# Kernel optimization log

Hardware: AMD Instinct MI355X
Metric: run time of the kernel (lower is better)

## Reference

```python
import jax, jax.numpy as jnp
import numpy as np

KERNEL = (3, 3, 3)
STRIDE = (1, 1, 1)
PAD = (1, 1, 1)
DIL = (1, 1, 1)


def setup_inputs() -> dict:
    key = jax.random.key(0)
    k1, k2 = jax.random.split(key)
    # input: [B, C, D, H, W]
    x = jax.random.normal(k1, (2, 64, 16, 64, 64), dtype=jnp.float32)
    # per-pixel weights: [B, heads, weight_channels, kernel_volume, D_out, H_out, W_out]
    weight = jax.random.normal(k2, (2, 1, 16, 27, 16, 64, 64), dtype=jnp.float32)
    return {"x": x, "weight": weight}


def _aggregate(x, weight):
    # involution-style 3D local aggregation with zero padding.
    B, C, D, H, W = x.shape
    _, heads, wc, kvol, Do, Ho, Wo = weight.shape
    kd, kh, kw = KERNEL
    assert kvol == kd * kh * kw and C % wc == 0
    Q = C // wc  # channel-sharing groups: channel c uses weight channel c % wc
    xp = jnp.pad(x, ((0, 0), (0, 0), (PAD[0], PAD[0]), (PAD[1], PAD[1]), (PAD[2], PAD[2])))
    # channels laid out so that c = q*wc + r -> weight channel r == c % wc
    out = jnp.zeros((B, heads, Q, wc, Do, Ho, Wo), dtype=x.dtype)
    for ikd in range(kd):
        for ikh in range(kh):
            for ikw in range(kw):  # fixed small structural loop (27 taps)
                k = (ikd * kh + ikh) * kw + ikw
                d0 = ikd * DIL[0]
                h0 = ikh * DIL[1]
                w0 = ikw * DIL[2]
                x_k = xp[:, :,
                         d0:d0 + (Do - 1) * STRIDE[0] + 1:STRIDE[0],
                         h0:h0 + (Ho - 1) * STRIDE[1] + 1:STRIDE[1],
                         w0:w0 + (Wo - 1) * STRIDE[2] + 1:STRIDE[2]]
                x_k = x_k.reshape(B, Q, wc, Do, Ho, Wo)
                # [B,1,Q,wc,Do,Ho,Wo] * [B,heads,1,wc,Do,Ho,Wo]
                out = out + x_k[:, None] * weight[:, :, None, :, k]
    return out.reshape(B, heads * C, Do, Ho, Wo)


def reference(x, weight):
    return _aggregate(x, weight)
```

## Files before the change

### kernel.cpp

```cpp
#include <hip/hip_runtime.h>
#include <stdint.h>


#define NQ 4
typedef float f4_t __attribute__((ext_vector_type(4)));

#define BUF_FLOATS (4 * 18 * 64)
#define LDS_FLOATS (64 + 4 * BUF_FLOATS + 64)

__device__ __forceinline__ void async_copy16(const float* gsrc, float* ldst) {
    __builtin_amdgcn_global_load_lds(
        (const __attribute__((address_space(1))) uint32_t*)gsrc,
        (__attribute__((address_space(3))) uint32_t*)ldst, 16, 0, 0);
}

__global__ __launch_bounds__(256) void lconv_kernel(
    const float* __restrict__ x, const float* __restrict__ wt, float* __restrict__ out,
    const float* __restrict__ zp)
{
    __shared__ float lds_raw[LDS_FLOATS];

    const int tid = threadIdx.x;
    const int tw  = tid & 15;
    const int th  = tid >> 4;

    int bid = blockIdx.x;
    const int ho_tile = bid & 3;  bid >>= 2;
    const int a       = bid & 3;  bid >>= 2;
    const int c       = bid & 15; bid >>= 4;
    const int b       = bid;

    const int ho_base = ho_tile * 16;
    const int ho  = ho_base + th;
    const int wo0 = tw * 4;
    const int d0  = a * 4;

    const float* xbase = x + ((size_t)(b * 64 + c) * 16) * 4096;

    auto stage = [&](int d) {
        const int buf   = (d + 1) & 3;
        const bool dok  = ((unsigned)d < 16u);
        float* dbase    = &lds_raw[64 + buf * BUF_FLOATS];
        #pragma unroll
        for (int it = 0; it < 5; ++it) {
            const int i = it * 256 + tid;
            if (i < 1152) {
                const int row = i >> 4;
                const int seg = i & 15;
                const int q   = row / 18;
                const int hl  = row - q * 18;
                const int gh  = ho_base - 1 + hl;
                const bool ok = dok && ((unsigned)gh < 64u);
                const float* src = ok
                    ? (xbase + (size_t)q * 1048576 + (size_t)d * 4096 + (size_t)gh * 64 + seg * 4)
                    : (zp + seg * 4);
                async_copy16(src, dbase + i * 4);
            }
        }
    };

    stage(d0 - 1);
    stage(d0);
    stage(d0 + 1);
    __syncthreads();

    for (int dd4 = 0; dd4 < 4; ++dd4) {
        const int dout = d0 + dd4;
        if (dd4 < 3) stage(dout + 2);

        const float* wbase = wt + (((size_t)(b * 16 + c) * 27) * 16 + dout) * 4096
                                + (size_t)ho * 64 + wo0;

        float acc[NQ][4];
        #pragma unroll
        for (int q = 0; q < NQ; ++q)
            #pragma unroll
            for (int j = 0; j < 4; ++j) acc[q][j] = 0.f;

        #pragma unroll
        for (int dd = 0; dd < 3; ++dd) {
            const int buf = (dout + dd) & 3;
            const float* bbase = &lds_raw[64 + buf * BUF_FLOATS];
            #pragma unroll
            for (int dh = 0; dh < 3; ++dh) {
                float xv[NQ][6];
                #pragma unroll
                for (int q = 0; q < NQ; ++q) {
                    const float* r = bbase + (q * 18 + th + dh) * 64;
                    const f4_t m = *reinterpret_cast<const f4_t*>(r + wo0);
                    xv[q][0] = (tw > 0)  ? r[wo0 - 1] : 0.f;
                    xv[q][1] = m.x; xv[q][2] = m.y; xv[q][3] = m.z; xv[q][4] = m.w;
                    xv[q][5] = (tw < 15) ? r[wo0 + 4] : 0.f;
                }
                #pragma unroll
                for (int dw = 0; dw < 3; ++dw) {
                    const int k = (dd * 3 + dh) * 3 + dw;
                    const f4_t w4 = __builtin_nontemporal_load(
                        reinterpret_cast<const f4_t*>(wbase + (size_t)k * 65536));
                    #pragma unroll
                    for (int q = 0; q < NQ; ++q) {
                        acc[q][0] = fmaf(xv[q][0 + dw], w4.x, acc[q][0]);
                        acc[q][1] = fmaf(xv[q][1 + dw], w4.y, acc[q][1]);
                        acc[q][2] = fmaf(xv[q][2 + dw], w4.z, acc[q][2]);
                        acc[q][3] = fmaf(xv[q][3 + dw], w4.w, acc[q][3]);
                    }
                }
            }
        }

        #pragma unroll
        for (int q = 0; q < NQ; ++q) {
            float* orow = out + ((size_t)(b * 64 + q * 16 + c) * 16 + dout) * 4096
                              + (size_t)ho * 64 + wo0;
            f4_t rr; rr.x = acc[q][0]; rr.y = acc[q][1]; rr.z = acc[q][2]; rr.w = acc[q][3];
            __builtin_nontemporal_store(rr, reinterpret_cast<f4_t*>(orow));
        }

        __syncthreads();
    }
}

extern "C" void kernel_launch(void* const* d_in, const int* in_sizes, int n_in,
                              void* d_out, int out_size, void* d_ws, size_t ws_size,
                              hipStream_t stream) {
    const float* x  = (const float*)d_in[0];
    const float* wt = (const float*)d_in[1];
    float* out      = (float*)d_out;

    hipMemsetAsync(d_ws, 0, 4096, stream);

    dim3 grid(512), block(256);
    hipLaunchKernelGGL(lconv_kernel, grid, block, 0, stream, x, wt, out,
                       (const float*)d_ws);
}
```

Measured before the change: 63.36 us.

## Assign one output depth per block with double-buffered LDS and XCD-aware block mapping

Each block now computes a single output depth slice instead of four, raising the grid from 512 to 2048 blocks. The LDS ring shrinks from four buffers to two, so more blocks can be resident. Block indices are remapped so that consecutive block IDs spread (b, c) pairs across XCDs. The cost is that each x depth slice is loaded about three times instead of roughly 1.5 times, adding L2 and HBM traffic for x. Out-of-range depth taps are now skipped rather than computed against zero-filled slices.

Result: faster. 56.40 us (median of 2 runs) (-11.0%).

```diff
diff --git a/kernel.cpp b/kernel.cpp
--- a/kernel.cpp
+++ b/kernel.cpp
@@ -5,8 +5,8 @@
 #define NQ 4
 typedef float f4_t __attribute__((ext_vector_type(4)));
 
-#define BUF_FLOATS (4 * 18 * 64)
-#define LDS_FLOATS (64 + 4 * BUF_FLOATS + 64)
+#define BUF_FLOATS (NQ * 18 * 64)
+#define LDS_FLOATS (16 + 2 * BUF_FLOATS + 16)
 
 __device__ __forceinline__ void async_copy16(const float* gsrc, float* ldst) {
     __builtin_amdgcn_global_load_lds(
@@ -18,69 +18,65 @@
     const float* __restrict__ x, const float* __restrict__ wt, float* __restrict__ out,
     const float* __restrict__ zp)
 {
-    __shared__ float lds_raw[LDS_FLOATS];
+    __shared__ __align__(16) float lds_raw[LDS_FLOATS];
 
     const int tid = threadIdx.x;
     const int tw  = tid & 15;
     const int th  = tid >> 4;
 
-    int bid = blockIdx.x;
-    const int ho_tile = bid & 3;  bid >>= 2;
-    const int a       = bid & 3;  bid >>= 2;
-    const int c       = bid & 15; bid >>= 4;
-    const int b       = bid;
+    const int bid  = blockIdx.x;
+    const int slot = bid >> 3;
+    const int bc   = (bid & 7) * 4 + (slot >> 6);
+    const int dout = (slot >> 2) & 15;
+    const int ho_tile = slot & 3;
+    const int b = bc >> 4, c = bc & 15;
 
     const int ho_base = ho_tile * 16;
     const int ho  = ho_base + th;
     const int wo0 = tw * 4;
-    const int d0  = a * 4;
 
     const float* xbase = x + ((size_t)(b * 64 + c) * 16) * 4096;
 
-    auto stage = [&](int d) {
-        const int buf   = (d + 1) & 3;
-        const bool dok  = ((unsigned)d < 16u);
-        float* dbase    = &lds_raw[64 + buf * BUF_FLOATS];
+    auto stage = [&](int buf, int d) {
+        float* dbase = &lds_raw[16 + buf * BUF_FLOATS];
         #pragma unroll
         for (int it = 0; it < 5; ++it) {
             const int i = it * 256 + tid;
-            if (i < 1152) {
+            if (it < 4 || i < 1152) {
                 const int row = i >> 4;
                 const int seg = i & 15;
                 const int q   = row / 18;
                 const int hl  = row - q * 18;
                 const int gh  = ho_base - 1 + hl;
-                const bool ok = dok && ((unsigned)gh < 64u);
-                const float* src = ok
-                    ? (xbase + (size_t)q * 1048576 + (size_t)d * 4096 + (size_t)gh * 64 + seg * 4)
+                const float* src = ((unsigned)gh < 64u)
+                    ? (xbase + (size_t)q * 1048576 + (size_t)d * 4096
+                             + (size_t)gh * 64 + seg * 4)
                     : (zp + seg * 4);
-                async_copy16(src, dbase + i * 4);
+                async_copy16(src, dbase + (size_t)i * 4);
             }
         }
     };
 
-    stage(d0 - 1);
-    stage(d0);
-    stage(d0 + 1);
+    float acc[NQ][4];
+    #pragma unroll
+    for (int q = 0; q < NQ; ++q)
+        #pragma unroll
+        for (int j = 0; j < 4; ++j) acc[q][j] = 0.f;
+
+    const float* wbase = wt + (((size_t)(b * 16 + c) * 27) * 16 + dout) * 4096
+                            + (size_t)ho * 64 + wo0;
+
+    if (dout > 0) stage(0, dout - 1);
     __syncthreads();
 
-    for (int dd4 = 0; dd4 < 4; ++dd4) {
-        const int dout = d0 + dd4;
-        if (dd4 < 3) stage(dout + 2);
+    #pragma unroll
+    for (int dd = 0; dd < 3; ++dd) {
+        const int cur = dd & 1, nxt = cur ^ 1;
+        if (dd < 2 && dout + dd < 16) stage(nxt, dout + dd);
 
-        const float* wbase = wt + (((size_t)(b * 16 + c) * 27) * 16 + dout) * 4096
-                                + (size_t)ho * 64 + wo0;
-
-        float acc[NQ][4];
-        #pragma unroll
-        for (int q = 0; q < NQ; ++q)
-            #pragma unroll
-            for (int j = 0; j < 4; ++j) acc[q][j] = 0.f;
-
-        #pragma unroll
-        for (int dd = 0; dd < 3; ++dd) {
-            const int buf = (dout + dd) & 3;
-            const float* bbase = &lds_raw[64 + buf * BUF_FLOATS];
+        const int d = dout + dd - 1;
+        if ((unsigned)d < 16u) {
+            const float* bbase = &lds_raw[16 + cur * BUF_FLOATS];
             #pragma unroll
             for (int dh = 0; dh < 3; ++dh) {
                 float xv[NQ][6];
@@ -88,9 +84,11 @@
                 for (int q = 0; q < NQ; ++q) {
                     const float* r = bbase + (q * 18 + th + dh) * 64;
                     const f4_t m = *reinterpret_cast<const f4_t*>(r + wo0);
-                    xv[q][0] = (tw > 0)  ? r[wo0 - 1] : 0.f;
+                    const float xl = r[wo0 - 1];
+                    const float xr = r[wo0 + 4];
+                    xv[q][0] = (tw > 0)  ? xl : 0.f;
                     xv[q][1] = m.x; xv[q][2] = m.y; xv[q][3] = m.z; xv[q][4] = m.w;
-                    xv[q][5] = (tw < 15) ? r[wo0 + 4] : 0.f;
+                    xv[q][5] = (tw < 15) ? xr : 0.f;
                 }
                 #pragma unroll
                 for (int dw = 0; dw < 3; ++dw) {
@@ -107,16 +105,15 @@
                 }
             }
         }
+        if (dd < 2) __syncthreads();
+    }
 
-        #pragma unroll
-        for (int q = 0; q < NQ; ++q) {
-            float* orow = out + ((size_t)(b * 64 + q * 16 + c) * 16 + dout) * 4096
-                              + (size_t)ho * 64 + wo0;
-            f4_t rr; rr.x = acc[q][0]; rr.y = acc[q][1]; rr.z = acc[q][2]; rr.w = acc[q][3];
-            __builtin_nontemporal_store(rr, reinterpret_cast<f4_t*>(orow));
-        }
-
-        __syncthreads();
+    #pragma unroll
+    for (int q = 0; q < NQ; ++q) {
+        float* orow = out + ((size_t)(b * 64 + q * 16 + c) * 16 + dout) * 4096
+                          + (size_t)ho * 64 + wo0;
+        f4_t rr; rr.x = acc[q][0]; rr.y = acc[q][1]; rr.z = acc[q][2]; rr.w = acc[q][3];
+        __builtin_nontemporal_store(rr, reinterpret_cast<f4_t*>(orow));
     }
 }
 
@@ -129,7 +126,7 @@
 
     hipMemsetAsync(d_ws, 0, 4096, stream);
 
-    dim3 grid(512), block(256);
+    dim3 grid(2048), block(256);
     hipLaunchKernelGGL(lconv_kernel, grid, block, 0, stream, x, wt, out,
                        (const float*)d_ws);
 }
```
